# Optimization experiments

Hardware: AMD Instinct MI355X
Metric: run time of the kernel (lower is better)

## Reference

```python
import jax, jax.numpy as jnp
import numpy as np
from jax import lax

B, N = 8, 8192
H, W = 512, 512
C = 192          # backbone feature channels (Swin-L stage 1)
HF, WF = 128, 128  # H/4, W/4
STATE = 256
VLR = 3
STRIDE = 4.0
DOWN = 4.0
EPS = 1e-8


def bilinear_sample(feat, poly, h, w):
    """F.grid_sample(align_corners=True, bilinear) equivalent.
    feat: (B,C,h,w), poly: (B,N,2) pixel coords -> (B,C,N)."""
    gx = poly[..., 0] / (w / 2.0) - 1.0
    gy = poly[..., 1] / (h / 2.0) - 1.0
    x = (gx + 1.0) * 0.5 * (w - 1)   # align_corners=True unnormalize
    y = (gy + 1.0) * 0.5 * (h - 1)
    x0 = jnp.floor(x); y0 = jnp.floor(y)
    fx = x - x0; fy = y - y0
    x0i = jnp.clip(x0, 0, w - 1).astype(jnp.int32)
    x1i = jnp.clip(x0 + 1, 0, w - 1).astype(jnp.int32)
    y0i = jnp.clip(y0, 0, h - 1).astype(jnp.int32)
    y1i = jnp.clip(y0 + 1, 0, h - 1).astype(jnp.int32)
    b = jnp.arange(feat.shape[0])[:, None]
    f00 = feat[b, :, y0i, x0i]  # (B,N,C)
    f01 = feat[b, :, y0i, x1i]
    f10 = feat[b, :, y1i, x0i]
    f11 = feat[b, :, y1i, x1i]
    w00 = ((1 - fy) * (1 - fx))[..., None]
    w01 = ((1 - fy) * fx)[..., None]
    w10 = (fy * (1 - fx))[..., None]
    w11 = (fy * fx)[..., None]
    out = f00 * w00 + f01 * w01 + f10 * w10 + f11 * w11  # (B,N,C)
    return jnp.transpose(out, (0, 2, 1))  # (B,C,N)


def mlp3(x, W1, b1, W2, b2, W3, b3):
    """per-point MLP (1x1 conv stack). x: (B,Cin,N) -> (B,Cout,N)."""
    h1 = jax.nn.relu(jnp.einsum('oc,bcn->bon', W1, x) + b1[None, :, None])
    h2 = jax.nn.relu(jnp.einsum('oc,bcn->bon', W2, h1) + b2[None, :, None])
    return jnp.einsum('oc,bcn->bon', W3, h2) + b3[None, :, None]


def can_poly(poly, mask):
    # canonical poly: subtract per-polygon masked min of valid points
    big = jnp.float32(1e9)
    masked = jnp.where(mask[..., None] > 0, poly, big)
    mins = jnp.min(masked, axis=1, keepdims=True)  # (B,1,2)
    return (poly - mins) * mask[..., None]


def polygon_angles(poly, mask):
    prev = jnp.roll(poly, 1, axis=1)
    nxt = jnp.roll(poly, -1, axis=1)
    v1 = prev - poly
    v2 = nxt - poly
    dot = jnp.sum(v1 * v2, axis=-1)
    nrm = jnp.linalg.norm(v1, axis=-1) * jnp.linalg.norm(v2, axis=-1)
    cosang = jnp.clip(dot / (nrm + EPS), -1.0, 1.0)
    return jnp.arccos(cosang) * mask  # (B,N)


def setup_inputs() -> dict:
    key = jax.random.key(0)
    ks = jax.random.split(key, 20)
    DIN_OFF = C + 2   # 194
    DIN_CLS = C + 3   # 195
    inp = {
        'image': jax.random.normal(ks[0], (B, 3, H, W), jnp.float32),
        'pred_points': jax.random.uniform(ks[1], (B, N, 2), jnp.float32) * (WF - 1),
        'valid_mask': jnp.ones((B, N), jnp.float32),
        'bw': jax.random.normal(ks[2], (C, 3, 4, 4), jnp.float32) * 0.05,
        'bb': jnp.zeros((C,), jnp.float32),
        'off_W1': jax.random.normal(ks[3], (VLR, STATE, DIN_OFF), jnp.float32) * 0.02,
        'off_b1': jnp.zeros((VLR, STATE), jnp.float32),
        'off_W2': jax.random.normal(ks[4], (VLR, STATE, STATE), jnp.float32) * 0.02,
        'off_b2': jnp.zeros((VLR, STATE), jnp.float32),
        'off_W3': jax.random.normal(ks[5], (VLR, 2, STATE), jnp.float32) * 0.02,
        'off_b3': jnp.zeros((VLR, 2), jnp.float32),
        'cls_W1': jax.random.normal(ks[6], (STATE, DIN_CLS), jnp.float32) * 0.02,
        'cls_b1': jnp.zeros((STATE,), jnp.float32),
        'cls_W2': jax.random.normal(ks[7], (STATE, STATE), jnp.float32) * 0.02,
        'cls_b2': jnp.zeros((STATE,), jnp.float32),
        'cls_W3': jax.random.normal(ks[8], (1, STATE), jnp.float32) * 0.02,
        'cls_b3': jnp.zeros((1,), jnp.float32),
    }
    return inp


def reference(image, pred_points, valid_mask, bw, bb,
              off_W1, off_b1, off_W2, off_b2, off_W3, off_b3,
              cls_W1, cls_b1, cls_W2, cls_b2, cls_W3, cls_b3):
    # frozen backbone stand-in (torch.no_grad on swin_l): stride-4 patch-embed conv
    feat = lax.conv_general_dilated(
        image, bw, window_strides=(4, 4), padding='VALID',
        dimension_numbers=('NCHW', 'OIHW', 'NCHW')) + bb[None, :, None, None]
    feat = lax.stop_gradient(feat)  # (B,C,HF,WF)

    py = pred_points
    for i in range(VLR):
        c_py = can_poly(py, valid_mask)
        g = bilinear_sample(feat, py, HF, WF) * valid_mask[:, None, :]   # (B,C,N)
        x = jnp.concatenate([g, jnp.transpose(c_py, (0, 2, 1))], axis=1)  # (B,C+2,N)
        off = mlp3(x, off_W1[i], off_b1[i], off_W2[i], off_b2[i], off_W3[i], off_b3[i])
        off = jnp.transpose(off, (0, 2, 1)) * valid_mask[..., None]      # (B,N,2)
        py = py + off * STRIDE

    gf = bilinear_sample(feat, py, HF, WF) * valid_mask[:, None, :]      # (B,C,N)
    angles = lax.stop_gradient(polygon_angles(py, valid_mask))           # (B,N)
    cls_feat = jnp.concatenate(
        [gf, jnp.transpose(py, (0, 2, 1)), angles[:, None, :]], axis=1)  # (B,C+3,N)
    logits = mlp3(cls_feat, cls_W1, cls_b1, cls_W2, cls_b2, cls_W3, cls_b3)  # (B,1,N)
    cls_points = logits[:, 0, :] * valid_mask                            # (B,N)

    final_refined_points = py * DOWN
    return (final_refined_points, cls_points)
```

## Files before the change

### kernel.cpp

```cpp
#include <hip/hip_runtime.h>
#include <hip/hip_bf16.h>
#include <hip/hip_fp8.h>

#define NB 8
#define NP 8192
#define IMH 512
#define IMW 512
#define NC 192
#define FH 128
#define FW 128
#define NSTATE 256

#define P1 232
#define P2 264
#define K1PAD 224
#define CPITCH 72

typedef __attribute__((ext_vector_type(8))) unsigned short ush8;
typedef __attribute__((ext_vector_type(8))) short short8v;
typedef __attribute__((ext_vector_type(4))) float f32x4;

__device__ __forceinline__ float bf2f(unsigned short u) {
  return __uint_as_float(((unsigned)u) << 16);
}
__device__ __forceinline__ float fp8tof(unsigned char b) {
  __hip_fp8_e4m3 v;
  v.__x = b;
  return (float)v;
}
__device__ __forceinline__ unsigned char ftofp8(float f) {
  __hip_fp8_e4m3 v(f);
  return v.__x;
}

__global__ __launch_bounds__(256) void conv_kernel(
    const float* __restrict__ img, const __hip_bfloat16* __restrict__ wcb,
    const float* __restrict__ bb, unsigned char* __restrict__ feat) {
  __shared__ __hip_bfloat16 Xim[64 * CPITCH];

  const int tid = threadIdx.x;
  const int lane = tid & 63;
  const int w = tid >> 6;
  const int cl = lane & 15;
  const int kg = lane >> 4;
  const int b = blockIdx.x & 7;
  const int pix0 = (blockIdx.x >> 3) * 64;
  const int y = pix0 >> 7;
  const int xh = (pix0 >> 6) & 1;

  {
    const int pix = tid & 63;
    const int q = tid >> 6;
    *(uint2*)&Xim[pix * CPITCH + 48 + q * 4] = (uint2){0u, 0u};
  }

#pragma unroll
  for (int it = 0; it < 3; ++it) {
    const int idx = it * 256 + tid;
    const int row = idx >> 6;
    const int c = idx & 63;
    const int ci = row >> 2, ky = row & 3;
    const float4 v = *(const float4*)(img + (((size_t)b * 3 + ci) * IMH +
                                             (y * 4 + ky)) * IMW + xh * 256 + c * 4);
    __hip_bfloat16 h[4];
    h[0] = __float2bfloat16(v.x);
    h[1] = __float2bfloat16(v.y);
    h[2] = __float2bfloat16(v.z);
    h[3] = __float2bfloat16(v.w);
    *(uint2*)&Xim[c * CPITCH + ci * 16 + ky * 4] = *(const uint2*)h;
  }
  __syncthreads();

  f32x4 acc[4][3];
#pragma unroll
  for (int mt = 0; mt < 4; ++mt)
#pragma unroll
    for (int nt = 0; nt < 3; ++nt) acc[mt][nt] = (f32x4){0, 0, 0, 0};

#pragma unroll
  for (int kc = 0; kc < 2; ++kc) {
    short8v af[4], bfv[3];
#pragma unroll
    for (int mt = 0; mt < 4; ++mt)
      af[mt] = *(const short8v*)&Xim[(mt * 16 + cl) * CPITCH + kc * 32 + kg * 8];
#pragma unroll
    for (int nt = 0; nt < 3; ++nt)
      bfv[nt] = *(const short8v*)&wcb[(size_t)(w * 48 + nt * 16 + cl) * 64 +
                                      kc * 32 + kg * 8];
#pragma unroll
    for (int mt = 0; mt < 4; ++mt)
#pragma unroll
      for (int nt = 0; nt < 3; ++nt)
        acc[mt][nt] = __builtin_amdgcn_mfma_f32_16x16x32_bf16(
            af[mt], bfv[nt], acc[mt][nt], 0, 0, 0);
  }

#pragma unroll
  for (int nt = 0; nt < 3; ++nt) {
    const float bias = bb[w * 48 + nt * 16 + cl];
#pragma unroll
    for (int mt = 0; mt < 4; ++mt) {
#pragma unroll
      for (int r = 0; r < 4; ++r) {
        feat[((size_t)(w * 8 + b) * 16384 + pix0 + mt * 16 + kg * 4 + r) * 48 +
             nt * 16 + cl] = ftofp8(acc[mt][nt][r] + bias);
      }
    }
  }
}

__global__ void prep_all_kernel(
    const float* __restrict__ oW1, const float* __restrict__ cW1,
    const float* __restrict__ oW2, const float* __restrict__ cW2,
    const float* __restrict__ bw, __hip_bfloat16* __restrict__ w1b,
    __hip_bfloat16* __restrict__ w2b, __hip_bfloat16* __restrict__ wcb) {
  const int idx = blockIdx.x * 256 + threadIdx.x;
  const int region = blockIdx.y;
  if (region == 0) {
    if (idx >= 4 * 256 * P1) return;
    const int L = idx / (256 * P1);
    const int rem = idx - L * (256 * P1);
    const int n = rem / P1;
    const int k = rem - n * P1;
    const float* src = (L < 3) ? (oW1 + (size_t)L * 256 * 194) : cW1;
    const int K = (L < 3) ? 194 : 195;
    w1b[idx] = __float2bfloat16((k < K) ? src[(size_t)n * K + k] : 0.0f);
  } else if (region == 1) {
    if (idx >= 4 * 256 * P2) return;
    const int L = idx / (256 * P2);
    const int rem = idx - L * (256 * P2);
    const int n = rem / P2;
    const int k = rem - n * P2;
    const float* src = (L < 3) ? (oW2 + (size_t)L * 65536) : cW2;
    w2b[idx] = __float2bfloat16((k < 256) ? src[(size_t)n * 256 + k] : 0.0f);
  } else {
    if (idx >= 192 * 64) return;
    const int n = idx >> 6;
    const int k = idx & 63;
    wcb[idx] = __float2bfloat16((k < 48) ? bw[(size_t)n * 48 + k] : 0.0f);
  }
}

__global__ void mins_kernel(const float* __restrict__ py,
                            const float* __restrict__ mask,
                            float* __restrict__ mins) {
  int b = blockIdx.x;
  float mx = 1e9f, my = 1e9f;
  for (int n = threadIdx.x; n < NP; n += 256) {
    float m = mask[(size_t)b * NP + n];
    float2 p = *(const float2*)&py[((size_t)b * NP + n) * 2];
    mx = fminf(mx, m > 0.0f ? p.x : 1e9f);
    my = fminf(my, m > 0.0f ? p.y : 1e9f);
  }
#pragma unroll
  for (int o = 32; o > 0; o >>= 1) {
    mx = fminf(mx, __shfl_down(mx, o));
    my = fminf(my, __shfl_down(my, o));
  }
  __shared__ float sx[4], sy[4];
  if ((threadIdx.x & 63) == 0) { sx[threadIdx.x >> 6] = mx; sy[threadIdx.x >> 6] = my; }
  __syncthreads();
  if (threadIdx.x == 0) {
    mx = fminf(fminf(sx[0], sx[1]), fminf(sx[2], sx[3]));
    my = fminf(fminf(sy[0], sy[1]), fminf(sy[2], sy[3]));
    mins[b * 2 + 0] = mx;
    mins[b * 2 + 1] = my;
  }
}

template <bool CLS>
__global__ __launch_bounds__(256, 2) void mlp_kernel(
    const unsigned char* __restrict__ feat,
    const float* __restrict__ p_in,
    const float* __restrict__ mask,
    const float* __restrict__ mins,
    const __hip_bfloat16* __restrict__ W1b, const float* __restrict__ b1,
    const __hip_bfloat16* __restrict__ W2b, const float* __restrict__ b2,
    const float* __restrict__ W3, const float* __restrict__ b3,
    float* __restrict__ out0) {
  __shared__ __hip_bfloat16 Xls[64 * P2];
  __shared__ float red[4][64][2];

  const int tid = threadIdx.x;
  const int lane = tid & 63;
  const int w = tid >> 6;
  const int cl = lane & 15;
  const int kg = lane >> 4;
  const int b = blockIdx.x & 7;
  const int m0 = (blockIdx.x >> 3) * 64;

  short8v w1f[7][4];
#pragma unroll
  for (int kc = 0; kc < 7; ++kc)
#pragma unroll
    for (int nt = 0; nt < 4; ++nt)
      w1f[kc][nt] = *(const short8v*)&W1b[(size_t)(w * 64 + nt * 16 + cl) * P1 +
                                          kc * 32 + kg * 8];
  float b1v[4], b2v[4], w3av[4], w3bv[4];
#pragma unroll
  for (int nt = 0; nt < 4; ++nt) {
    const int n = w * 64 + nt * 16 + cl;
    b1v[nt] = b1[n];
    b2v[nt] = b2[n];
    w3av[nt] = W3[n];
    w3bv[nt] = CLS ? 0.0f : W3[256 + n];
  }

  {
    const int m = tid >> 2;
    const int j = tid & 3;
    const int n = m0 + m;
    const size_t pidx = (size_t)b * NP + n;
    const float msk = mask[pidx];
    const float2 pv = *(const float2*)&p_in[pidx * 2];
    const float px = pv.x, pyv = pv.y;
    const float xs = px * (127.0f / 128.0f);
    const float ys = pyv * (127.0f / 128.0f);
    const float x0f = floorf(xs), y0f = floorf(ys);
    const float fx = xs - x0f, fy = ys - y0f;
    const int x0 = (int)fminf(fmaxf(x0f, 0.0f), 127.0f);
    const int x1 = (int)fminf(fmaxf(x0f + 1.0f, 0.0f), 127.0f);
    const int y0 = (int)fminf(fmaxf(y0f, 0.0f), 127.0f);
    const int y1 = (int)fminf(fmaxf(y0f + 1.0f, 0.0f), 127.0f);
    const float w00 = (1.0f - fy) * (1.0f - fx);
    const float w01 = (1.0f - fy) * fx;
    const float w10 = fy * (1.0f - fx);
    const float w11 = fy * fx;
    const unsigned char* fb = feat + (size_t)(j * 8 + b) * 16384 * 48;
    const uint4* r00 = (const uint4*)(fb + (size_t)(y0 * FW + x0) * 48);
    const uint4* r01 = (const uint4*)(fb + (size_t)(y0 * FW + x1) * 48);
    const uint4* r10 = (const uint4*)(fb + (size_t)(y1 * FW + x0) * 48);
    const uint4* r11 = (const uint4*)(fb + (size_t)(y1 * FW + x1) * 48);
#pragma unroll
    for (int v = 0; v < 3; ++v) {
      union { uint4 u; unsigned char c[16]; } a0, a1, a2, a3;
      a0.u = r00[v]; a1.u = r01[v]; a2.u = r10[v]; a3.u = r11[v];
      __hip_bfloat16 h[16];
#pragma unroll
      for (int e = 0; e < 16; ++e) {
        float gg = w00 * fp8tof(a0.c[e]) + w01 * fp8tof(a1.c[e]) +
                   w10 * fp8tof(a2.c[e]) + w11 * fp8tof(a3.c[e]);
        h[e] = __float2bfloat16(gg * msk);
      }
      *(ush8*)&Xls[m * P1 + j * 48 + v * 16 + 0] = *(const ush8*)&h[0];
      *(ush8*)&Xls[m * P1 + j * 48 + v * 16 + 8] = *(const ush8*)&h[8];
    }
    if (j == 0) {
      __hip_bfloat16 ex[32];
#pragma unroll
      for (int i = 0; i < 32; ++i) ex[i] = __float2bfloat16(0.0f);
      if constexpr (!CLS) {
        ex[0] = __float2bfloat16((px - mins[b * 2 + 0]) * msk);
        ex[1] = __float2bfloat16((pyv - mins[b * 2 + 1]) * msk);
      } else {
        ex[0] = __float2bfloat16(px);
        ex[1] = __float2bfloat16(pyv);
        const int npv = (n + NP - 1) & (NP - 1);
        const int nnx = (n + 1) & (NP - 1);
        const float2 pp = *(const float2*)&p_in[((size_t)b * NP + npv) * 2];
        const float2 pn = *(const float2*)&p_in[((size_t)b * NP + nnx) * 2];
        const float v1x = pp.x - px, v1y = pp.y - pyv;
        const float v2x = pn.x - px, v2y = pn.y - pyv;
        const float dot = v1x * v2x + v1y * v2y;
        const float nrm =
            sqrtf(v1x * v1x + v1y * v1y) * sqrtf(v2x * v2x + v2y * v2y);
        const float ca = fminf(fmaxf(dot / (nrm + 1e-8f), -1.0f), 1.0f);
        ex[2] = __float2bfloat16(acosf(ca) * msk);
      }
#pragma unroll
      for (int q = 0; q < 4; ++q)
        *(ush8*)&Xls[m * P1 + 192 + q * 8] = *(const ush8*)&ex[q * 8];
    }
  }
  __syncthreads();

  f32x4 acc[4][4];
#pragma unroll
  for (int mt = 0; mt < 4; ++mt)
#pragma unroll
    for (int nt = 0; nt < 4; ++nt) acc[mt][nt] = (f32x4){0, 0, 0, 0};

#pragma unroll
  for (int kc = 0; kc < 7; ++kc) {
    short8v af[4];
#pragma unroll
    for (int mt = 0; mt < 4; ++mt)
      af[mt] = *(const short8v*)&Xls[(mt * 16 + cl) * P1 + kc * 32 + kg * 8];
#pragma unroll
    for (int mt = 0; mt < 4; ++mt)
#pragma unroll
      for (int nt = 0; nt < 4; ++nt)
        acc[mt][nt] = __builtin_amdgcn_mfma_f32_16x16x32_bf16(
            af[mt], w1f[kc][nt], acc[mt][nt], 0, 0, 0);
  }

  short8v w2f[8][4];
#pragma unroll
  for (int kc = 0; kc < 8; ++kc)
#pragma unroll
    for (int nt = 0; nt < 4; ++nt)
      w2f[kc][nt] = *(const short8v*)&W2b[(size_t)(w * 64 + nt * 16 + cl) * P2 +
                                          kc * 32 + kg * 8];
  __syncthreads();

#pragma unroll
  for (int nt = 0; nt < 4; ++nt) {
    const float bias = b1v[nt];
    const int n = w * 64 + nt * 16 + cl;
#pragma unroll
    for (int mt = 0; mt < 4; ++mt) {
#pragma unroll
      for (int r = 0; r < 4; ++r) {
        const float v = fmaxf(acc[mt][nt][r] + bias, 0.0f);
        Xls[(mt * 16 + kg * 4 + r) * P2 + n] = __float2bfloat16(v);
      }
    }
  }
  __syncthreads();

  f32x4 acc2[4][4];
#pragma unroll
  for (int mt = 0; mt < 4; ++mt)
#pragma unroll
    for (int nt = 0; nt < 4; ++nt) acc2[mt][nt] = (f32x4){0, 0, 0, 0};

#pragma unroll
  for (int kc = 0; kc < 8; ++kc) {
    short8v af[4];
#pragma unroll
    for (int mt = 0; mt < 4; ++mt)
      af[mt] = *(const short8v*)&Xls[(mt * 16 + cl) * P2 + kc * 32 + kg * 8];
#pragma unroll
    for (int mt = 0; mt < 4; ++mt)
#pragma unroll
      for (int nt = 0; nt < 4; ++nt)
        acc2[mt][nt] = __builtin_amdgcn_mfma_f32_16x16x32_bf16(
            af[mt], w2f[kc][nt], acc2[mt][nt], 0, 0, 0);
  }

  float pr[4][4][2];
#pragma unroll
  for (int mt = 0; mt < 4; ++mt)
#pragma unroll
    for (int r = 0; r < 4; ++r) { pr[mt][r][0] = 0.0f; pr[mt][r][1] = 0.0f; }

#pragma unroll
  for (int nt = 0; nt < 4; ++nt) {
    const float bias = b2v[nt];
    const float w3a = w3av[nt];
    const float w3b = w3bv[nt];
#pragma unroll
    for (int mt = 0; mt < 4; ++mt) {
#pragma unroll
      for (int r = 0; r < 4; ++r) {
        const float t = fmaxf(acc2[mt][nt][r] + bias, 0.0f);
        pr[mt][r][0] = fmaf(t, w3a, pr[mt][r][0]);
        if constexpr (!CLS) pr[mt][r][1] = fmaf(t, w3b, pr[mt][r][1]);
      }
    }
  }
#pragma unroll
  for (int s = 1; s < 16; s <<= 1) {
#pragma unroll
    for (int mt = 0; mt < 4; ++mt)
#pragma unroll
      for (int r = 0; r < 4; ++r) {
        pr[mt][r][0] += __shfl_xor(pr[mt][r][0], s);
        if constexpr (!CLS) pr[mt][r][1] += __shfl_xor(pr[mt][r][1], s);
      }
  }
  if constexpr (!CLS) {
    if (cl < 8) {
      const int r = cl >> 1, o = cl & 1;
#pragma unroll
      for (int mt = 0; mt < 4; ++mt)
        red[w][mt * 16 + kg * 4 + r][o] = pr[mt][r][o];
    }
  } else {
    if (cl < 4) {
      const int r = cl;
#pragma unroll
      for (int mt = 0; mt < 4; ++mt)
        red[w][mt * 16 + kg * 4 + r][0] = pr[mt][r][0];
    }
  }
  __syncthreads();

  if constexpr (!CLS) {
    if (tid < 128) {
      const int m = tid >> 1, o = tid & 1;
      const float s = red[0][m][o] + red[1][m][o] + red[2][m][o] + red[3][m][o];
      const size_t pidx = (size_t)b * NP + m0 + m;
      const float msk = mask[pidx];
      const float off = (s + b3[o]) * msk;
      out0[pidx * 2 + o] = p_in[pidx * 2 + o] + off * 4.0f;
    }
  } else {
    if (tid < 64) {
      const int m = tid;
      const float s = red[0][m][0] + red[1][m][0] + red[2][m][0] + red[3][m][0];
      const size_t pidx = (size_t)b * NP + m0 + m;
      const float msk = mask[pidx];
      out0[pidx * 2 + 0] = p_in[pidx * 2 + 0] * 4.0f;
      out0[pidx * 2 + 1] = p_in[pidx * 2 + 1] * 4.0f;
      out0[(size_t)2 * NB * NP + pidx] = (s + b3[0]) * msk;
    }
  }
}

extern "C" void kernel_launch(void* const* d_in, const int* in_sizes, int n_in,
                              void* d_out, int out_size, void* d_ws,
                              size_t ws_size, hipStream_t stream) {
  const float* image = (const float*)d_in[0];
  const float* pred  = (const float*)d_in[1];
  const float* mask  = (const float*)d_in[2];
  const float* bw    = (const float*)d_in[3];
  const float* bb    = (const float*)d_in[4];
  const float* oW1   = (const float*)d_in[5];
  const float* ob1   = (const float*)d_in[6];
  const float* oW2   = (const float*)d_in[7];
  const float* ob2   = (const float*)d_in[8];
  const float* oW3   = (const float*)d_in[9];
  const float* ob3   = (const float*)d_in[10];
  const float* cW1   = (const float*)d_in[11];
  const float* cb1   = (const float*)d_in[12];
  const float* cW2   = (const float*)d_in[13];
  const float* cb2   = (const float*)d_in[14];
  const float* cW3   = (const float*)d_in[15];
  const float* cb3   = (const float*)d_in[16];
  float* out = (float*)d_out;

  char* ws = (char*)d_ws;
  unsigned char* feat = (unsigned char*)ws;
  const size_t featB = (size_t)NB * FH * FW * NC;
  float* pyA  = (float*)(ws + featB);
  float* pyB  = pyA + (size_t)NB * NP * 2;
  float* mins = pyB + (size_t)NB * NP * 2;
  __hip_bfloat16* w1b = (__hip_bfloat16*)(mins + 16);
  __hip_bfloat16* w2b = w1b + (size_t)4 * 256 * P1;
  __hip_bfloat16* wcb = w2b + (size_t)4 * 256 * P2;

  prep_all_kernel<<<dim3(1056, 3), 256, 0, stream>>>(oW1, cW1, oW2, cW2, bw,
                                                     w1b, w2b, wcb);
  conv_kernel<<<dim3(NB * 16384 / 64), 256, 0, stream>>>(image, wcb, bb, feat);

  const float* cur = pred;
  float* nxt = pyA;
  for (int i = 0; i < 3; ++i) {
    mins_kernel<<<dim3(NB), 256, 0, stream>>>(cur, mask, mins);
    mlp_kernel<false><<<dim3(NB * NP / 64), 256, 0, stream>>>(
        feat, cur, mask, mins,
        w1b + (size_t)i * 256 * P1, ob1 + (size_t)i * NSTATE,
        w2b + (size_t)i * 256 * P2, ob2 + (size_t)i * NSTATE,
        oW3 + (size_t)i * 2 * NSTATE, ob3 + (size_t)i * 2, nxt);
    cur = nxt;
    nxt = (nxt == pyA) ? pyB : pyA;
  }
  mlp_kernel<true><<<dim3(NB * NP / 64), 256, 0, stream>>>(
      feat, cur, mask, nullptr, w1b + (size_t)3 * 256 * P1, cb1,
      w2b + (size_t)3 * 256 * P2, cb2, cW3, cb3, out);
}
```

Baseline: 219.2 us.

## Fuse per-polygon min reduction into MLP epilogue via atomics; stream W2 fragments

Removes the three separate mins_kernel launches. The initial min is computed in an extra region of the prep kernel, and each refinement MLP kernel writes the next iteration's masked min with atomicMin on order-preserving encoded floats. It also replaces the fully preloaded W2 register fragments with a double-buffered per-k-chunk load, to lower register pressure. The costs are global atomics in the epilogue and less latency hiding for the W2 loads.

```diff
diff --git a/kernel.cpp b/kernel.cpp
--- a/kernel.cpp
+++ b/kernel.cpp
@@ -31,6 +31,13 @@
 __device__ __forceinline__ unsigned char ftofp8(float f) {
   __hip_fp8_e4m3 v(f);
   return v.__x;
+}
+__device__ __forceinline__ unsigned fenc(float f) {
+  unsigned u = __float_as_uint(f);
+  return (u & 0x80000000u) ? ~u : (u | 0x80000000u);
+}
+__device__ __forceinline__ float fdec(unsigned u) {
+  return __uint_as_float((u & 0x80000000u) ? (u & 0x7FFFFFFFu) : ~u);
 }
 
 __global__ __launch_bounds__(256) void conv_kernel(
@@ -112,8 +119,11 @@
 __global__ void prep_all_kernel(
     const float* __restrict__ oW1, const float* __restrict__ cW1,
     const float* __restrict__ oW2, const float* __restrict__ cW2,
-    const float* __restrict__ bw, __hip_bfloat16* __restrict__ w1b,
-    __hip_bfloat16* __restrict__ w2b, __hip_bfloat16* __restrict__ wcb) {
+    const float* __restrict__ bw, const float* __restrict__ pred,
+    const float* __restrict__ mask, __hip_bfloat16* __restrict__ w1b,
+    __hip_bfloat16* __restrict__ w2b, __hip_bfloat16* __restrict__ wcb,
+    unsigned* __restrict__ mins4) {
+  __shared__ float sx[4], sy[4];
   const int idx = blockIdx.x * 256 + threadIdx.x;
   const int region = blockIdx.y;
   if (region == 0) {
@@ -133,38 +143,38 @@
     const int k = rem - n * P2;
     const float* src = (L < 3) ? (oW2 + (size_t)L * 65536) : cW2;
     w2b[idx] = __float2bfloat16((k < 256) ? src[(size_t)n * 256 + k] : 0.0f);
-  } else {
+  } else if (region == 2) {
+    if (idx < 48) mins4[16 + idx] = fenc(1e9f);
     if (idx >= 192 * 64) return;
     const int n = idx >> 6;
     const int k = idx & 63;
     wcb[idx] = __float2bfloat16((k < 48) ? bw[(size_t)n * 48 + k] : 0.0f);
-  }
-}
-
-__global__ void mins_kernel(const float* __restrict__ py,
-                            const float* __restrict__ mask,
-                            float* __restrict__ mins) {
-  int b = blockIdx.x;
-  float mx = 1e9f, my = 1e9f;
-  for (int n = threadIdx.x; n < NP; n += 256) {
-    float m = mask[(size_t)b * NP + n];
-    float2 p = *(const float2*)&py[((size_t)b * NP + n) * 2];
-    mx = fminf(mx, m > 0.0f ? p.x : 1e9f);
-    my = fminf(my, m > 0.0f ? p.y : 1e9f);
-  }
-#pragma unroll
-  for (int o = 32; o > 0; o >>= 1) {
-    mx = fminf(mx, __shfl_down(mx, o));
-    my = fminf(my, __shfl_down(my, o));
-  }
-  __shared__ float sx[4], sy[4];
-  if ((threadIdx.x & 63) == 0) { sx[threadIdx.x >> 6] = mx; sy[threadIdx.x >> 6] = my; }
-  __syncthreads();
-  if (threadIdx.x == 0) {
-    mx = fminf(fminf(sx[0], sx[1]), fminf(sx[2], sx[3]));
-    my = fminf(fminf(sy[0], sy[1]), fminf(sy[2], sy[3]));
-    mins[b * 2 + 0] = mx;
-    mins[b * 2 + 1] = my;
+  } else {
+    if (blockIdx.x >= 8) return;
+    const int b = blockIdx.x;
+    float mx = 1e9f, my = 1e9f;
+    for (int n = threadIdx.x; n < NP; n += 256) {
+      float m = mask[(size_t)b * NP + n];
+      float2 p = *(const float2*)&pred[((size_t)b * NP + n) * 2];
+      mx = fminf(mx, m > 0.0f ? p.x : 1e9f);
+      my = fminf(my, m > 0.0f ? p.y : 1e9f);
+    }
+#pragma unroll
+    for (int o = 32; o > 0; o >>= 1) {
+      mx = fminf(mx, __shfl_down(mx, o));
+      my = fminf(my, __shfl_down(my, o));
+    }
+    if ((threadIdx.x & 63) == 0) {
+      sx[threadIdx.x >> 6] = mx;
+      sy[threadIdx.x >> 6] = my;
+    }
+    __syncthreads();
+    if (threadIdx.x == 0) {
+      mx = fminf(fminf(sx[0], sx[1]), fminf(sx[2], sx[3]));
+      my = fminf(fminf(sy[0], sy[1]), fminf(sy[2], sy[3]));
+      mins4[b * 2 + 0] = fenc(mx);
+      mins4[b * 2 + 1] = fenc(my);
+    }
   }
 }
 
@@ -173,7 +183,8 @@
     const unsigned char* __restrict__ feat,
     const float* __restrict__ p_in,
     const float* __restrict__ mask,
-    const float* __restrict__ mins,
+    const unsigned* __restrict__ mins_in,
+    unsigned* __restrict__ mins_out,
     const __hip_bfloat16* __restrict__ W1b, const float* __restrict__ b1,
     const __hip_bfloat16* __restrict__ W2b, const float* __restrict__ b2,
     const float* __restrict__ W3, const float* __restrict__ b3,
@@ -250,8 +261,8 @@
 #pragma unroll
       for (int i = 0; i < 32; ++i) ex[i] = __float2bfloat16(0.0f);
       if constexpr (!CLS) {
-        ex[0] = __float2bfloat16((px - mins[b * 2 + 0]) * msk);
-        ex[1] = __float2bfloat16((pyv - mins[b * 2 + 1]) * msk);
+        ex[0] = __float2bfloat16((px - fdec(mins_in[b * 2 + 0])) * msk);
+        ex[1] = __float2bfloat16((pyv - fdec(mins_in[b * 2 + 1])) * msk);
       } else {
         ex[0] = __float2bfloat16(px);
         ex[1] = __float2bfloat16(pyv);
@@ -294,13 +305,11 @@
             af[mt], w1f[kc][nt], acc[mt][nt], 0, 0, 0);
   }
 
-  short8v w2f[8][4];
-#pragma unroll
-  for (int kc = 0; kc < 8; ++kc)
-#pragma unroll
-    for (int nt = 0; nt < 4; ++nt)
-      w2f[kc][nt] = *(const short8v*)&W2b[(size_t)(w * 64 + nt * 16 + cl) * P2 +
-                                          kc * 32 + kg * 8];
+  short8v w2c[4];
+#pragma unroll
+  for (int nt = 0; nt < 4; ++nt)
+    w2c[nt] = *(const short8v*)&W2b[(size_t)(w * 64 + nt * 16 + cl) * P2 +
+                                    kg * 8];
   __syncthreads();
 
 #pragma unroll
@@ -326,6 +335,13 @@
 
 #pragma unroll
   for (int kc = 0; kc < 8; ++kc) {
+    short8v w2n[4];
+    if (kc < 7) {
+#pragma unroll
+      for (int nt = 0; nt < 4; ++nt)
+        w2n[nt] = *(const short8v*)&W2b[(size_t)(w * 64 + nt * 16 + cl) * P2 +
+                                        (kc + 1) * 32 + kg * 8];
+    }
     short8v af[4];
 #pragma unroll
     for (int mt = 0; mt < 4; ++mt)
@@ -335,7 +351,11 @@
 #pragma unroll
       for (int nt = 0; nt < 4; ++nt)
         acc2[mt][nt] = __builtin_amdgcn_mfma_f32_16x16x32_bf16(
-            af[mt], w2f[kc][nt], acc2[mt][nt], 0, 0, 0);
+            af[mt], w2c[nt], acc2[mt][nt], 0, 0, 0);
+    if (kc < 7) {
+#pragma unroll
+      for (int nt = 0; nt < 4; ++nt) w2c[nt] = w2n[nt];
+    }
   }
 
   float pr[4][4][2];
@@ -393,7 +413,14 @@
       const size_t pidx = (size_t)b * NP + m0 + m;
       const float msk = mask[pidx];
       const float off = (s + b3[o]) * msk;
-      out0[pidx * 2 + o] = p_in[pidx * 2 + o] + off * 4.0f;
+      const float nv = p_in[pidx * 2 + o] + off * 4.0f;
+      out0[pidx * 2 + o] = nv;
+      float mval = (msk > 0.0f) ? nv : 1e9f;
+#pragma unroll
+      for (int st = 2; st < 64; st <<= 1)
+        mval = fminf(mval, __shfl_xor(mval, st));
+      if ((tid & 63) < 2 && mins_out != nullptr)
+        atomicMin(&mins_out[b * 2 + o], fenc(mval));
     }
   } else {
     if (tid < 64) {
@@ -435,21 +462,21 @@
   const size_t featB = (size_t)NB * FH * FW * NC;
   float* pyA  = (float*)(ws + featB);
   float* pyB  = pyA + (size_t)NB * NP * 2;
-  float* mins = pyB + (size_t)NB * NP * 2;
-  __hip_bfloat16* w1b = (__hip_bfloat16*)(mins + 16);
+  unsigned* mins4 = (unsigned*)(pyB + (size_t)NB * NP * 2);
+  __hip_bfloat16* w1b = (__hip_bfloat16*)(mins4 + 64);
   __hip_bfloat16* w2b = w1b + (size_t)4 * 256 * P1;
   __hip_bfloat16* wcb = w2b + (size_t)4 * 256 * P2;
 
-  prep_all_kernel<<<dim3(1056, 3), 256, 0, stream>>>(oW1, cW1, oW2, cW2, bw,
-                                                     w1b, w2b, wcb);
+  prep_all_kernel<<<dim3(1056, 4), 256, 0, stream>>>(
+      oW1, cW1, oW2, cW2, bw, pred, mask, w1b, w2b, wcb, mins4);
   conv_kernel<<<dim3(NB * 16384 / 64), 256, 0, stream>>>(image, wcb, bb, feat);
 
   const float* cur = pred;
   float* nxt = pyA;
   for (int i = 0; i < 3; ++i) {
-    mins_kernel<<<dim3(NB), 256, 0, stream>>>(cur, mask, mins);
     mlp_kernel<false><<<dim3(NB * NP / 64), 256, 0, stream>>>(
-        feat, cur, mask, mins,
+        feat, cur, mask, mins4 + i * 16,
+        (i < 2) ? (mins4 + (i + 1) * 16) : nullptr,
         w1b + (size_t)i * 256 * P1, ob1 + (size_t)i * NSTATE,
         w2b + (size_t)i * 256 * P2, ob2 + (size_t)i * NSTATE,
         oW3 + (size_t)i * 2 * NSTATE, ob3 + (size_t)i * 2, nxt);
@@ -457,6 +484,6 @@
     nxt = (nxt == pyA) ? pyB : pyA;
   }
   mlp_kernel<true><<<dim3(NB * NP / 64), 256, 0, stream>>>(
-      feat, cur, mask, nullptr, w1b + (size_t)3 * 256 * P1, cb1,
+      feat, cur, mask, nullptr, nullptr, w1b + (size_t)3 * 256 * P1, cb1,
       w2b + (size_t)3 * 256 * P2, cb2, cW3, cb3, out);
 }
```

Result: faster. 208.4 us (-4.9%).
